# Kernel optimization log

Hardware: AMD Instinct MI355X
Metric: run time of the kernel (lower is better)

## Reference

```python
import jax, jax.numpy as jnp
import numpy as np
import math

K = 20; M = 10; N = K * M; DEG = N - 1; AJR = 30; HID = 96
NH = 4; HD = HID + 2 + K; DM = NH * HD  # 472


def _graph():
    # complete graph: node i receives edges from all j != i (fixed in-degree DEG)
    idx = jnp.arange(N)
    j = jnp.arange(DEG)
    srcs = jnp.where(j[None, :] < idx[:, None], j[None, :], j[None, :] + 1)  # [N, DEG]
    grp = idx // M
    same = (grp[srcs] == grp[:, None]).astype(jnp.float32)  # e_type[:,1]
    return srcs, same


def _pe_table(max_step, dim):
    pos = np.arange(max_step)[:, None].astype(np.float32)
    div = np.exp(np.arange(0, dim, 2).astype(np.float32) * -(math.log(10000.0) / dim))
    pe = np.zeros((max_step, dim), np.float32)
    pe[:, 0::2] = np.sin(pos * div)
    pe[:, 1::2] = np.cos(pos * div)
    return jnp.asarray(pe)


def _gcn(h, x, label, w, d, srcs, same, p):
    (l0w, l0b, l1w, l1b, l2w, l2b, l3w, l3b, l4w, l4b, l5w, l5b) = p
    t0 = 1.0 - same
    h_src = h[srcs]                      # [N, DEG, HID] gather
    we = w[..., None]
    n1_v = (h_src * we * t0[..., None]).sum(1) / (w * t0).sum(1, keepdims=True)
    n2_v = (h_src * we * same[..., None]).sum(1) / (w * same).sum(1, keepdims=True)
    n1_e = jnp.sort(d * t0, axis=1)[:, ::-1][:, :AJR]      # top-AJR cross-group dists
    n2_e = jnp.sort(d * same, axis=1)[:, ::-1][:, :M - 1]  # top-(m-1) same-group dists
    return jax.nn.relu(x @ l0w + l0b + label @ l1w + l1b + n1_v @ l2w + l2b
                       + n2_v @ l3w + l3b + n1_e @ l4w + l4b + n2_e @ l5w + l5b)


def _forward(x, label, h0, w, d,
             l0_w, l0_b, l1_w, l1_b, l2_w, l2_b, l3_w, l3_b, l4_w, l4_b, l5_w, l5_b,
             mha_w0, mha_b0, mha_w1, mha_b1, mha_w3, mha_b3,
             v1_w, v1_b, v2_w, v2_b, gnn_step, max_step, remain_step):
    srcs, same = _graph()
    gcn_p = (l0_w, l0_b, l1_w, l1_b, l2_w, l2_b, l3_w, l3_b, l4_w, l4_b, l5_w, l5_b)
    h = h0
    for _ in range(gnn_step):
        h = _gcn(h, x, label, w, d, srcs, same, gcn_p)
    pe = _pe_table(max_step, HID)
    h_full = jnp.concatenate([h + pe[remain_step], x, label], axis=1)  # [N, HD]
    gc = h_full.T @ label / M                                          # [HD, K]
    kv = jnp.tile(h_full, (1, NH))                                     # [N, DM]
    kh = (kv @ mha_w0 + mha_b0).reshape(N, NH, HD).transpose(1, 0, 2)  # keys use linears[0]
    vh = (kv @ mha_w1 + mha_b1).reshape(N, NH, HD).transpose(1, 0, 2)  # values use linears[1]
    h_rep = jnp.repeat(h_full, N, axis=0)      # torch repeat(1,n).view(n*n, hd)
    h_tile = jnp.tile(h_full, (N, 1))          # torch repeat(n,1)
    la_rep = jnp.repeat(label, N, axis=0) @ gc.T
    la_tile = jnp.tile(label, (N, 1)) @ gc.T
    Q1 = jnp.concatenate([h_rep, h_tile, la_rep, la_tile], axis=1)  # [N*N, DM]
    Q2 = jnp.concatenate([h_tile, h_rep, la_tile, la_rep], axis=1)
    inv_sqrt_dk = 1.0 / jnp.sqrt(jnp.float32(HD))

    def attend(Q):
        q = (Q @ mha_w0 + mha_b0).reshape(-1, NH, HD)
        s = jnp.einsum('bhd,hkd->bhk', q, kh) * inv_sqrt_dk
        p = jax.nn.softmax(s, axis=-1)
        o = jnp.einsum('bhk,hkd->bhd', p, vh).reshape(-1, DM)
        return o @ mha_w3 + mha_b3

    S = attend(Q1) + attend(Q2)               # [N*N, DM]
    S_a_encoding = S[:, None, :]              # [N*N, 1, DM]
    Q_sa = (jax.nn.relu(S @ v1_w + v1_b) @ v2_w + v2_b).squeeze()  # [N*N]
    return S_a_encoding, h, h_full, Q_sa


def setup_inputs() -> dict:
    key = jax.random.key(0)
    ks = jax.random.split(key, 32)
    def rn(i, shape, s=1.0):
        return jax.random.normal(ks[i], shape, jnp.float32) * s
    grp = jnp.arange(N) // M
    label = jax.nn.one_hot(grp, K, dtype=jnp.float32)
    return {
        'x': rn(0, (N, 2)),
        'label': label,
        'h0': rn(1, (N, HID)),
        'w': jax.random.uniform(ks[2], (N, DEG), jnp.float32, 0.1, 1.0),
        'd': jax.random.uniform(ks[3], (N, DEG), jnp.float32, 0.0, 1.0),
        'l0_w': rn(4, (2, HID), 0.5), 'l0_b': rn(5, (HID,), 0.05),
        'l1_w': rn(6, (K, HID), 0.2), 'l1_b': rn(7, (HID,), 0.05),
        'l2_w': rn(8, (HID, HID), 0.1), 'l2_b': rn(9, (HID,), 0.05),
        'l3_w': rn(10, (HID, HID), 0.1), 'l3_b': rn(11, (HID,), 0.05),
        'l4_w': rn(12, (AJR, HID), 0.15), 'l4_b': rn(13, (HID,), 0.05),
        'l5_w': rn(14, (M - 1, HID), 0.3), 'l5_b': rn(15, (HID,), 0.05),
        'mha_w0': rn(16, (DM, DM), 0.04), 'mha_b0': rn(17, (DM,), 0.02),
        'mha_w1': rn(18, (DM, DM), 0.04), 'mha_b1': rn(19, (DM,), 0.02),
        'mha_w3': rn(20, (DM, DM), 0.04), 'mha_b3': rn(21, (DM,), 0.02),
        'v1_w': rn(22, (DM, HID // 2), 0.04), 'v1_b': rn(23, (HID // 2,), 0.02),
        'v2_w': rn(24, (HID // 2, 1), 0.1), 'v2_b': rn(25, (1,), 0.02),
        'gnn_step': 2, 'max_step': 50, 'remain_step': 10,
    }


def reference(x, label, h0, w, d,
              l0_w, l0_b, l1_w, l1_b, l2_w, l2_b, l3_w, l3_b, l4_w, l4_b, l5_w, l5_b,
              mha_w0, mha_b0, mha_w1, mha_b1, mha_w3, mha_b3,
              v1_w, v1_b, v2_w, v2_b, gnn_step, max_step, remain_step):
    return _forward(x, label, h0, w, d,
                    l0_w, l0_b, l1_w, l1_b, l2_w, l2_b, l3_w, l3_b, l4_w, l4_b, l5_w, l5_b,
                    mha_w0, mha_b0, mha_w1, mha_b1, mha_w3, mha_b3,
                    v1_w, v1_b, v2_w, v2_b, gnn_step, max_step, remain_step)
```

## Files before the change

kernel.cpp:

```cpp
#include <hip/hip_runtime.h>
#include <hip/hip_bf16.h>
#include <math.h>

typedef unsigned short ushort;
typedef unsigned int uint;

#define NV 200
#define DEG 199
#define HID 96
#define KG 20
#define MG 10
#define AJR 30
#define NH 4
#define HD 118
#define DM 472
#define NN 40000
#define NT 20100
#define NTP 20160

#define WS_BASE   0
#define WS_H1     19200
#define WS_H2     38400
#define WS_HFULL  57600
#define WS_GMEAN  81200
#define WS_KHF    194952
#define WS_VHF    289352
#define WS_B1     383752
#define WS_B2     478152
#define WS_SC1    572552
#define WS_SC2    732552
#define WS_ZT     1315464

#define OFF_H   18880000
#define OFF_HF  18899200
#define OFF_Q   18922800

typedef __attribute__((ext_vector_type(8))) short short8v;
typedef __attribute__((ext_vector_type(4))) float float4v;

__device__ __forceinline__ ushort f2bf(float f) {
  uint u = __float_as_uint(f);
  uint r = (u + 0x7fffu + ((u >> 16) & 1u)) >> 16;
  return (ushort)r;
}
__device__ __forceinline__ uint packbf(float a, float b) {
  __hip_bfloat162 h2 = __float22bfloat162_rn(make_float2(a, b));
  union { __hip_bfloat162 h; uint u; } c;
  c.h = h2;
  return c.u;
}

__device__ __forceinline__ int triOff(int i) {
  return i * 200 - ((i * (i - 1)) >> 1);
}
__device__ __forceinline__ void p2ij(int p, int& io, int& jo) {
  float s = sqrtf((float)(160801 - 8 * p));
  int i = (int)((401.0f - s) * 0.5f);
  if (i < 0) i = 0;
  if (i > 199) i = 199;
  while (i > 0 && triOff(i) > p) --i;
  while (i < 199 && triOff(i + 1) <= p) ++i;
  io = i;
  jo = i + (p - triOff(i));
}

__global__ __launch_bounds__(256) void k_base(
    const float* __restrict__ x, const float* __restrict__ dmat,
    const float* __restrict__ label,
    const float* __restrict__ l0w, const float* __restrict__ l0b,
    const float* __restrict__ l1w, const float* __restrict__ l1b,
    const float* __restrict__ l2b, const float* __restrict__ l3b,
    const float* __restrict__ l4w, const float* __restrict__ l4b,
    const float* __restrict__ l5w, const float* __restrict__ l5b,
    float* __restrict__ base) {
  int i = blockIdx.x; int t = threadIdx.x;
  int g = i / MG;
  __shared__ float sv[256];
  __shared__ float sn2[9];
  float v = -1.0f;
  if (t < DEG) {
    int u = (t < i) ? t : t + 1;
    if (u / MG != g) v = dmat[i * DEG + t];
  }
  sv[t] = v;
  __syncthreads();
  for (int k2 = 2; k2 <= 256; k2 <<= 1) {
    for (int jj = k2 >> 1; jj > 0; jj >>= 1) {
      int ixj = t ^ jj;
      if (ixj > t) {
        float a = sv[t], b = sv[ixj];
        bool sw = ((t & k2) == 0) ? (a < b) : (a > b);
        if (sw) { sv[t] = b; sv[ixj] = a; }
      }
      __syncthreads();
    }
  }
  if (t == 0) {
    float tmp[9];
    for (int q = 0; q < 9; q++) tmp[q] = dmat[i * DEG + MG * g + q];
    for (int a2 = 1; a2 < 9; a2++) {
      float key = tmp[a2]; int b2 = a2 - 1;
      while (b2 >= 0 && tmp[b2] < key) { tmp[b2 + 1] = tmp[b2]; b2--; }
      tmp[b2 + 1] = key;
    }
    for (int q = 0; q < 9; q++) sn2[q] = tmp[q];
  }
  __syncthreads();
  if (t < HID) {
    float acc = l0b[t] + l1b[t] + l2b[t] + l3b[t] + l4b[t] + l5b[t];
    acc += x[i * 2 + 0] * l0w[t] + x[i * 2 + 1] * l0w[HID + t];
    for (int k = 0; k < KG; k++) acc += label[i * KG + k] * l1w[k * HID + t];
    for (int q = 0; q < AJR; q++) acc += sv[q] * l4w[q * HID + t];
    for (int q = 0; q < 9; q++) acc += sn2[q] * l5w[q * HID + t];
    base[i * HID + t] = acc;
  }
}

__global__ __launch_bounds__(256) void k_gcn2(
    const float* __restrict__ hin, const float* __restrict__ base,
    const float* __restrict__ w, const float* __restrict__ l2w,
    const float* __restrict__ l3w, float* __restrict__ hout) {
  int i = blockIdx.x; int t = threadIdx.x;
  int g = i / MG;
  __shared__ float pA[HID], wA[HID], pB[HID], wB[HID];
  __shared__ float n1s[HID], n2s[HID];
  __shared__ float m0[HID], m1[HID];
  if (t < HID) {
    float acc = 0.f, ws = 0.f;
    for (int j = 0; j < 100; j++) {
      int u = (j < i) ? j : j + 1;
      if (u / MG != g) {
        float wj = w[i * DEG + j];
        acc += wj * hin[u * HID + t];
        ws += wj;
      }
    }
    pA[t] = acc; wA[t] = ws;
  } else if (t < 2 * HID) {
    int dd = t - HID;
    float acc = 0.f, ws = 0.f;
    for (int j = 100; j < DEG; j++) {
      int u = (j < i) ? j : j + 1;
      if (u / MG != g) {
        float wj = w[i * DEG + j];
        acc += wj * hin[u * HID + dd];
        ws += wj;
      }
    }
    pB[dd] = acc; wB[dd] = ws;
  } else if (t < 224) {
#pragma unroll
    for (int q = 0; q < 3; q++) {
      int dd = (t - 192) * 3 + q;
      float acc = 0.f, ws = 0.f;
      for (int u = MG * g; u < MG * g + MG; u++) {
        if (u == i) continue;
        int j = (u < i) ? u : u - 1;
        float wj = w[i * DEG + j];
        acc += wj * hin[u * HID + dd];
        ws += wj;
      }
      n2s[dd] = acc / ws;
    }
  }
  __syncthreads();
  if (t < HID) n1s[t] = (pA[t] + pB[t]) / (wA[t] + wB[t]);
  __syncthreads();
  if (t < HID) {
    float acc = 0.f;
    for (int dd = 0; dd < 48; dd++)
      acc += n1s[dd] * l2w[dd * HID + t] + n2s[dd] * l3w[dd * HID + t];
    m0[t] = acc;
  } else if (t < 2 * HID) {
    int c = t - HID;
    float acc = 0.f;
    for (int dd = 48; dd < HID; dd++)
      acc += n1s[dd] * l2w[dd * HID + c] + n2s[dd] * l3w[dd * HID + c];
    m1[c] = acc;
  }
  __syncthreads();
  if (t < HID)
    hout[i * HID + t] = fmaxf(base[i * HID + t] + m0[t] + m1[t], 0.f);
}

__global__ __launch_bounds__(128) void k_hfull(
    const float* __restrict__ h, const float* __restrict__ x,
    const float* __restrict__ label, const int* __restrict__ remain_step,
    float* __restrict__ hfull, float* __restrict__ out_h,
    float* __restrict__ out_hf) {
  int i = blockIdx.x; int t = threadIdx.x;
  if (t < HD) {
    float v;
    if (t < HID) {
      int p = *remain_step;
      int t2 = t & ~1;
      float div = expf(-(float)t2 * (logf(10000.f) / (float)HID));
      float ang = (float)p * div;
      float pe = (t & 1) ? cosf(ang) : sinf(ang);
      float hv = h[i * HID + t];
      out_h[i * HID + t] = hv;
      v = hv + pe;
    } else if (t < HID + 2) {
      v = x[i * 2 + (t - HID)];
    } else {
      v = label[i * KG + (t - HID - 2)];
    }
    hfull[i * HD + t] = v;
    out_hf[i * HD + t] = v;
  }
}

__global__ __launch_bounds__(128) void k_gmean(
    const float* __restrict__ hfull, float* __restrict__ gmean) {
  int g = blockIdx.x; int t = threadIdx.x;
  if (t < HD) {
    float s = 0.f;
    for (int q = 0; q < MG; q++) s += hfull[(g * MG + q) * HD + t];
    gmean[g * HD + t] = s * 0.1f;
  }
}

__global__ __launch_bounds__(256) void k_kvB(
    const float* __restrict__ hfull, const float* __restrict__ gmean,
    const float* __restrict__ w0, const float* __restrict__ b0v,
    const float* __restrict__ w1, const float* __restrict__ b1v,
    float* __restrict__ khfT, float* __restrict__ vhf,
    float* __restrict__ B1, float* __restrict__ B2) {
  int i = blockIdx.x; int t = threadIdx.x; int g = i / MG;
  int half = blockIdx.y;
  __shared__ float hr[HD], gr[HD];
  if (t < HD) { hr[t] = hfull[i * HD + t]; gr[t] = gmean[g * HD + t]; }
  __syncthreads();
  for (int c = half * 236 + t; c < 236 + half * 236; c += 256) {
    const float* w0c = w0 + c;
    const float* w1c = w1 + c;
    float d0 = 0.f, d1 = 0.f, d2 = 0.f, d3 = 0.f;
    float g2 = 0.f, g3 = 0.f;
    float e0 = 0.f, e1 = 0.f, e2 = 0.f, e3 = 0.f;
    for (int dd = 0; dd < HD; dd++) {
      float hv = hr[dd], gv = gr[dd];
      float a0 = w0c[dd * DM];
      float a1 = w0c[(HD + dd) * DM];
      float a2 = w0c[(2 * HD + dd) * DM];
      float a3 = w0c[(3 * HD + dd) * DM];
      d0 += hv * a0; d1 += hv * a1; d2 += hv * a2; d3 += hv * a3;
      g2 += gv * a2; g3 += gv * a3;
      e0 += hv * w1c[dd * DM];
      e1 += hv * w1c[(HD + dd) * DM];
      e2 += hv * w1c[(2 * HD + dd) * DM];
      e3 += hv * w1c[(3 * HD + dd) * DM];
    }
    float b0c = b0v[c];
    khfT[c * NV + i] = b0c + d0 + d1 + d2 + d3;
    vhf[i * DM + c] = b1v[c] + e0 + e1 + e2 + e3;
    B1[i * DM + c] = d0 + g2;
    B2[i * DM + c] = b0c + d1 + g3;
  }
}

__global__ __launch_bounds__(256) void k_SC(
    const float* __restrict__ B1, const float* __restrict__ B2,
    const float* __restrict__ khfT, float* __restrict__ SC1,
    float* __restrict__ SC2) {
  int i = blockIdx.x; int t = threadIdx.x;
  int half = blockIdx.y;
  const float scl = 1.4426950408889634f / sqrtf((float)HD);
  __shared__ float b1r[DM], b2r[DM];
  for (int c = t; c < DM; c += 256) { b1r[c] = B1[i * DM + c]; b2r[c] = B2[i * DM + c]; }
  __syncthreads();
  for (int p = half * 400 + t; p < half * 400 + 400; p += 256) {
    int h = p / NV, k = p - h * NV;
    float s1a = 0.f, s2a = 0.f;
    const float* kc = khfT + (size_t)h * HD * NV + k;
    const float* b1h = b1r + h * HD;
    const float* b2h = b2r + h * HD;
    for (int dd = 0; dd < HD; dd++) {
      float kv = kc[dd * NV];
      s1a += b1h[dd] * kv;
      s2a += b2h[dd] * kv;
    }
    SC1[h * NN + i * NV + k] = s1a * scl;
    SC2[h * NN + i * NV + k] = s2a * scl;
  }
}

__global__ __launch_bounds__(256) void k_ml(
    const float* __restrict__ SC1, const float* __restrict__ SC2,
    float* __restrict__ C) {
  int i = blockIdx.x, h = blockIdx.y;
  int t = threadIdx.x;
  __shared__ float s1s[224];
  for (int k = t; k < 224; k += 256)
    s1s[k] = (k < NV) ? SC1[h * NN + i * NV + k] : -1e30f;
  __syncthreads();
  int l = t & 31;
  int g = t >> 5;
  const float* s2b = SC2 + h * NN;
  for (int it = 0; it < 25; ++it) {
    int j = it * 8 + g;
    const float* row = s2b + j * NV;
    float v[7];
#pragma unroll
    for (int e = 0; e < 7; ++e) {
      int k = l + 32 * e;
      v[e] = (k < NV) ? (s1s[k] + row[k]) : -1e30f;
    }
    float m = v[0];
#pragma unroll
    for (int e = 1; e < 7; ++e) m = fmaxf(m, v[e]);
#pragma unroll
    for (int off = 16; off > 0; off >>= 1) m = fmaxf(m, __shfl_xor(m, off, 32));
    float s = 0.f;
#pragma unroll
    for (int e = 0; e < 7; ++e) s += exp2f(v[e] - m);
#pragma unroll
    for (int off = 16; off > 0; off >>= 1) s += __shfl_xor(s, off, 32);
    if (l == 0) C[h * NN + i * NV + j] = m + log2f(s);
  }
}

__global__ __launch_bounds__(256) void k_ZZT(
    const float* __restrict__ vhf, const float* __restrict__ w3,
    ushort* __restrict__ ZT) {
  int k = blockIdx.x, h = blockIdx.y;
  int t = threadIdx.x;
  __shared__ float vr[HD];
  if (k < NV && t < HD) vr[t] = vhf[k * DM + h * HD + t];
  __syncthreads();
  for (int c = t; c < 512; c += 256) {
    float a = 0.f;
    if (k < NV && c < DM) {
      for (int d = 0; d < HD; ++d) a += vr[d] * w3[(h * HD + d) * DM + c];
    }
    ZT[(size_t)c * 896 + h * 224 + k] = f2bf(a);
  }
}

__global__ __launch_bounds__(256) void k_sfusedT2(
    const float* __restrict__ SC1, const float* __restrict__ SC2,
    const float* __restrict__ C, const ushort* __restrict__ ZT,
    const float* __restrict__ b3, float* __restrict__ outS) {
  int t = threadIdx.x;
  int c0 = blockIdx.x * 128, p0 = blockIdx.y * 64;
  int lane = t & 63, wm = t >> 6;
  int frow = lane & 15, quad = lane >> 4;
  __shared__ __align__(16) ushort Bs[128 * 40];
  int p = p0 + wm * 16 + frow;
  bool bval = (p < NT);
  int iA = 0, jA = 0;
  if (bval) p2ij(p, iA, jA);
  int iN = iA * NV, jN = jA * NV;
  float4v acc[8];
#pragma unroll
  for (int n = 0; n < 8; ++n) acc[n] = (float4v)(0.f);
  int rB = t >> 1, khB = (t & 1) * 16;

  for (int h = 0; h < NH; ++h) {
    int hb = h * NN;
    const float* s1h = SC1 + hb;
    const float* s2h = SC2 + hb;
    float ci = bval ? C[hb + iN + jA] : 0.f;
    float cj = bval ? C[hb + jN + iA] : 0.f;
    for (int ks = 0; ks < 7; ++ks) {
      int kb = ks * 32 + quad * 8;
      bool kvalid = (kb + 7 < NV);
      union { uint4 q; short8v v; } af;
      if (bval && kvalid) {
        const float* q1i = s1h + iN + kb;
        const float* q2i = s2h + iN + kb;
        const float* q1j = s1h + jN + kb;
        const float* q2j = s2h + jN + kb;
        float4 a0 = *(const float4*)q1i,   a0b = *(const float4*)(q1i + 4);
        float4 b0 = *(const float4*)q2j,   b0b = *(const float4*)(q2j + 4);
        float4 d0 = *(const float4*)q1j,   d0b = *(const float4*)(q1j + 4);
        float4 e0 = *(const float4*)q2i,   e0b = *(const float4*)(q2i + 4);
        float p0_ = exp2f(a0.x + b0.x - ci) + exp2f(d0.x + e0.x - cj);
        float p1_ = exp2f(a0.y + b0.y - ci) + exp2f(d0.y + e0.y - cj);
        float p2_ = exp2f(a0.z + b0.z - ci) + exp2f(d0.z + e0.z - cj);
        float p3_ = exp2f(a0.w + b0.w - ci) + exp2f(d0.w + e0.w - cj);
        float p4_ = exp2f(a0b.x + b0b.x - ci) + exp2f(d0b.x + e0b.x - cj);
        float p5_ = exp2f(a0b.y + b0b.y - ci) + exp2f(d0b.y + e0b.y - cj);
        float p6_ = exp2f(a0b.z + b0b.z - ci) + exp2f(d0b.z + e0b.z - cj);
        float p7_ = exp2f(a0b.w + b0b.w - ci) + exp2f(d0b.w + e0b.w - cj);
        af.q.x = packbf(p0_, p1_);
        af.q.y = packbf(p2_, p3_);
        af.q.z = packbf(p4_, p5_);
        af.q.w = packbf(p6_, p7_);
      } else {
        af.q = make_uint4(0, 0, 0, 0);
      }
      const uint4* wp = (const uint4*)(ZT + (size_t)(c0 + rB) * 896 +
                                       h * 224 + ks * 32 + khB);
      uint4 bq0 = wp[0], bq1 = wp[1];
      __syncthreads();
      *(uint4*)&Bs[rB * 40 + khB] = bq0;
      *(uint4*)&Bs[rB * 40 + khB + 8] = bq1;
      __syncthreads();
#pragma unroll
      for (int n = 0; n < 8; ++n) {
        short8v bf = *(const short8v*)&Bs[(n * 16 + frow) * 40 + quad * 8];
        acc[n] = __builtin_amdgcn_mfma_f32_16x16x32_bf16(af.v, bf, acc[n],
                                                         0, 0, 0);
      }
    }
  }
  int ie[4], je[4];
#pragma unroll
  for (int r2 = 0; r2 < 4; ++r2) {
    int pe = p0 + wm * 16 + quad * 4 + r2;
    if (pe < NT) {
      p2ij(pe, ie[r2], je[r2]);
    } else {
      ie[r2] = -1; je[r2] = 0;
    }
  }
#pragma unroll
  for (int n = 0; n < 8; ++n) {
    int c = c0 + n * 16 + frow;
    if (c >= DM) continue;
    float bb = 2.0f * b3[c];
#pragma unroll
    for (int r2 = 0; r2 < 4; ++r2) {
      int ii = ie[r2];
      if (ii < 0) continue;
      int jj = je[r2];
      float v = acc[n][r2] + bb;
      outS[(size_t)(ii * NV + jj) * DM + c] = v;
      if (ii != jj) outS[(size_t)(jj * NV + ii) * DM + c] = v;
    }
  }
}

__global__ __launch_bounds__(256) void k_qsaT2(
    const float* __restrict__ S, const float* __restrict__ v1w,
    const float* __restrict__ v1b, const float* __restrict__ v2w,
    const float* __restrict__ v2b, float* __restrict__ outQ) {
  __shared__ float Ss[32][61];
  __shared__ float V1s[59][48];
  __shared__ float Ts[32][49];
  __shared__ int rowI[32], rowJ[32], rowOfs[32];
  int t = threadIdx.x;
  int p0b = blockIdx.x * 32;
  if (t < 32) {
    int p = p0b + t;
    if (p < NT) {
      int ii, jj; p2ij(p, ii, jj);
      rowI[t] = ii; rowJ[t] = jj; rowOfs[t] = ii * NV + jj;
    } else {
      rowI[t] = -1; rowJ[t] = 0; rowOfs[t] = 0;
    }
  }
  int ty2 = (t >> 4) * 2;
  int tx3 = (t & 15) * 3;
  float a00 = 0.f, a01 = 0.f, a02 = 0.f, a10 = 0.f, a11 = 0.f, a12 = 0.f;
  for (int k0 = 0; k0 < DM; k0 += 59) {
    __syncthreads();
    for (int e = t; e < 32 * 59; e += 256) {
      int r = e / 59, cc = e - r * 59;
      Ss[r][cc] = S[(size_t)rowOfs[r] * DM + k0 + cc];
    }
    for (int e = t; e < 59 * 48; e += 256) {
      int kk = e / 48, cc = e - kk * 48;
      V1s[kk][cc] = v1w[(size_t)(k0 + kk) * 48 + cc];
    }
    __syncthreads();
    for (int kk = 0; kk < 59; ++kk) {
      float s0 = Ss[ty2][kk], s1 = Ss[ty2 + 1][kk];
      float w0_ = V1s[kk][tx3], w1_ = V1s[kk][tx3 + 1], w2_ = V1s[kk][tx3 + 2];
      a00 += s0 * w0_; a01 += s0 * w1_; a02 += s0 * w2_;
      a10 += s1 * w0_; a11 += s1 * w1_; a12 += s1 * w2_;
    }
  }
  float b0 = v1b[tx3], b1 = v1b[tx3 + 1], b2 = v1b[tx3 + 2];
  Ts[ty2][tx3] = fmaxf(a00 + b0, 0.f);
  Ts[ty2][tx3 + 1] = fmaxf(a01 + b1, 0.f);
  Ts[ty2][tx3 + 2] = fmaxf(a02 + b2, 0.f);
  Ts[ty2 + 1][tx3] = fmaxf(a10 + b0, 0.f);
  Ts[ty2 + 1][tx3 + 1] = fmaxf(a11 + b1, 0.f);
  Ts[ty2 + 1][tx3 + 2] = fmaxf(a12 + b2, 0.f);
  __syncthreads();
  if (t < 32 && rowI[t] >= 0) {
    float q = v2b[0];
    for (int c = 0; c < 48; c++) q += Ts[t][c] * v2w[c];
    int ii = rowI[t], jj = rowJ[t];
    outQ[ii * NV + jj] = q;
    if (ii != jj) outQ[jj * NV + ii] = q;
  }
}

extern "C" void kernel_launch(void* const* d_in, const int* in_sizes, int n_in,
                              void* d_out, int out_size, void* d_ws,
                              size_t ws_size, hipStream_t stream) {
  const float* x = (const float*)d_in[0];
  const float* label = (const float*)d_in[1];
  const float* h0 = (const float*)d_in[2];
  const float* w = (const float*)d_in[3];
  const float* dmat = (const float*)d_in[4];
  const float* l0w = (const float*)d_in[5];
  const float* l0b = (const float*)d_in[6];
  const float* l1w = (const float*)d_in[7];
  const float* l1b = (const float*)d_in[8];
  const float* l2w = (const float*)d_in[9];
  const float* l2b = (const float*)d_in[10];
  const float* l3w = (const float*)d_in[11];
  const float* l3b = (const float*)d_in[12];
  const float* l4w = (const float*)d_in[13];
  const float* l4b = (const float*)d_in[14];
  const float* l5w = (const float*)d_in[15];
  const float* l5b = (const float*)d_in[16];
  const float* w0 = (const float*)d_in[17];
  const float* b0v = (const float*)d_in[18];
  const float* w1 = (const float*)d_in[19];
  const float* b1v = (const float*)d_in[20];
  const float* w3 = (const float*)d_in[21];
  const float* b3 = (const float*)d_in[22];
  const float* v1w = (const float*)d_in[23];
  const float* v1b = (const float*)d_in[24];
  const float* v2w = (const float*)d_in[25];
  const float* v2b = (const float*)d_in[26];
  const int* remain_step = (const int*)d_in[29];

  float* ws = (float*)d_ws;
  float* base = ws + WS_BASE;
  float* h1 = ws + WS_H1;
  float* h2 = ws + WS_H2;
  float* hfull = ws + WS_HFULL;
  float* gmean = ws + WS_GMEAN;
  float* khfT = ws + WS_KHF;
  float* vhf = ws + WS_VHF;
  float* B1 = ws + WS_B1;
  float* B2 = ws + WS_B2;
  float* SC1 = ws + WS_SC1;
  float* SC2 = ws + WS_SC2;
  ushort* ZT = (ushort*)(ws + WS_ZT);
  float* C = ws + WS_B1;

  float* outS = (float*)d_out;
  float* outH = outS + OFF_H;
  float* outHF = outS + OFF_HF;
  float* outQ = outS + OFF_Q;

  k_base<<<NV, 256, 0, stream>>>(x, dmat, label, l0w, l0b, l1w, l1b, l2b, l3b,
                                 l4w, l4b, l5w, l5b, base);
  k_gcn2<<<NV, 256, 0, stream>>>(h0, base, w, l2w, l3w, h1);
  k_gcn2<<<NV, 256, 0, stream>>>(h1, base, w, l2w, l3w, h2);
  k_hfull<<<NV, 128, 0, stream>>>(h2, x, label, remain_step, hfull, outH, outHF);
  k_gmean<<<KG, 128, 0, stream>>>(hfull, gmean);
  k_kvB<<<dim3(NV, 2), 256, 0, stream>>>(hfull, gmean, w0, b0v, w1, b1v, khfT,
                                         vhf, B1, B2);
  k_ZZT<<<dim3(224, NH), 256, 0, stream>>>(vhf, w3, ZT);
  k_SC<<<dim3(NV, 2), 256, 0, stream>>>(B1, B2, khfT, SC1, SC2);
  k_ml<<<dim3(NV, NH), 256, 0, stream>>>(SC1, SC2, C);
  k_sfusedT2<<<dim3(4, NTP / 64), 256, 0, stream>>>(SC1, SC2, C, ZT, b3, outS);
  k_qsaT2<<<(NT + 31) / 32, 256, 0, stream>>>(outS, v1w, v1b, v2w, v2b, outQ);
}
```

Baseline: 507.3 us.

## Widen fused attention-output tile and raise parallelism in small GCN/score kernels

The fused MFMA kernel now covers 256 output columns per block instead of 128. This halves how often each block recomputes the exp2-based bf16 probability A-fragments, at the cost of more accumulator registers and a larger shared tile. The GCN neighbour aggregation is split across 4 thread groups with 512-thread blocks. k_SC and k_ml get twice as many blocks by splitting their work ranges. The separate group-mean kernel is folded into k_kvB, which saves one launch but makes each block redundantly sum 10 rows.

```diff
diff --git a/kernel.cpp b/kernel.cpp
--- a/kernel.cpp
+++ b/kernel.cpp
@@ -22,7 +22,6 @@
 #define WS_H1     19200
 #define WS_H2     38400
 #define WS_HFULL  57600
-#define WS_GMEAN  81200
 #define WS_KHF    194952
 #define WS_VHF    289352
 #define WS_B1     383752
@@ -116,42 +115,33 @@
   }
 }
 
-__global__ __launch_bounds__(256) void k_gcn2(
+__global__ __launch_bounds__(512) void k_gcn4(
     const float* __restrict__ hin, const float* __restrict__ base,
     const float* __restrict__ w, const float* __restrict__ l2w,
     const float* __restrict__ l3w, float* __restrict__ hout) {
   int i = blockIdx.x; int t = threadIdx.x;
   int g = i / MG;
-  __shared__ float pA[HID], wA[HID], pB[HID], wB[HID];
+  __shared__ float pJ[4][HID], wJ[4][HID];
   __shared__ float n1s[HID], n2s[HID];
-  __shared__ float m0[HID], m1[HID];
-  if (t < HID) {
+  __shared__ float m[4][HID];
+  if (t < 384) {
+    int q = t / HID;
+    int c = t - q * HID;
+    int j0 = q * 50, j1 = (q == 3) ? DEG : (j0 + 50);
     float acc = 0.f, ws = 0.f;
-    for (int j = 0; j < 100; j++) {
+    for (int j = j0; j < j1; j++) {
       int u = (j < i) ? j : j + 1;
       if (u / MG != g) {
         float wj = w[i * DEG + j];
-        acc += wj * hin[u * HID + t];
+        acc += wj * hin[u * HID + c];
         ws += wj;
       }
     }
-    pA[t] = acc; wA[t] = ws;
-  } else if (t < 2 * HID) {
-    int dd = t - HID;
-    float acc = 0.f, ws = 0.f;
-    for (int j = 100; j < DEG; j++) {
-      int u = (j < i) ? j : j + 1;
-      if (u / MG != g) {
-        float wj = w[i * DEG + j];
-        acc += wj * hin[u * HID + dd];
-        ws += wj;
-      }
-    }
-    pB[dd] = acc; wB[dd] = ws;
-  } else if (t < 224) {
-#pragma unroll
-    for (int q = 0; q < 3; q++) {
-      int dd = (t - 192) * 3 + q;
+    pJ[q][c] = acc; wJ[q][c] = ws;
+  } else if (t < 416) {
+#pragma unroll
+    for (int q2 = 0; q2 < 3; q2++) {
+      int dd = (t - 384) * 3 + q2;
       float acc = 0.f, ws = 0.f;
       for (int u = MG * g; u < MG * g + MG; u++) {
         if (u == i) continue;
@@ -164,23 +154,22 @@
     }
   }
   __syncthreads();
-  if (t < HID) n1s[t] = (pA[t] + pB[t]) / (wA[t] + wB[t]);
-  __syncthreads();
-  if (t < HID) {
+  if (t < HID)
+    n1s[t] = (pJ[0][t] + pJ[1][t] + pJ[2][t] + pJ[3][t]) /
+             (wJ[0][t] + wJ[1][t] + wJ[2][t] + wJ[3][t]);
+  __syncthreads();
+  if (t < 384) {
+    int q = t / HID, c = t - q * HID;
+    int d0 = q * 24;
     float acc = 0.f;
-    for (int dd = 0; dd < 48; dd++)
-      acc += n1s[dd] * l2w[dd * HID + t] + n2s[dd] * l3w[dd * HID + t];
-    m0[t] = acc;
-  } else if (t < 2 * HID) {
-    int c = t - HID;
-    float acc = 0.f;
-    for (int dd = 48; dd < HID; dd++)
+    for (int dd = d0; dd < d0 + 24; dd++)
       acc += n1s[dd] * l2w[dd * HID + c] + n2s[dd] * l3w[dd * HID + c];
-    m1[c] = acc;
+    m[q][c] = acc;
   }
   __syncthreads();
   if (t < HID)
-    hout[i * HID + t] = fmaxf(base[i * HID + t] + m0[t] + m1[t], 0.f);
+    hout[i * HID + t] =
+        fmaxf(base[i * HID + t] + m[0][t] + m[1][t] + m[2][t] + m[3][t], 0.f);
 }
 
 __global__ __launch_bounds__(128) void k_hfull(
@@ -210,18 +199,8 @@
   }
 }
 
-__global__ __launch_bounds__(128) void k_gmean(
-    const float* __restrict__ hfull, float* __restrict__ gmean) {
-  int g = blockIdx.x; int t = threadIdx.x;
-  if (t < HD) {
-    float s = 0.f;
-    for (int q = 0; q < MG; q++) s += hfull[(g * MG + q) * HD + t];
-    gmean[g * HD + t] = s * 0.1f;
-  }
-}
-
 __global__ __launch_bounds__(256) void k_kvB(
-    const float* __restrict__ hfull, const float* __restrict__ gmean,
+    const float* __restrict__ hfull,
     const float* __restrict__ w0, const float* __restrict__ b0v,
     const float* __restrict__ w1, const float* __restrict__ b1v,
     float* __restrict__ khfT, float* __restrict__ vhf,
@@ -229,7 +208,12 @@
   int i = blockIdx.x; int t = threadIdx.x; int g = i / MG;
   int half = blockIdx.y;
   __shared__ float hr[HD], gr[HD];
-  if (t < HD) { hr[t] = hfull[i * HD + t]; gr[t] = gmean[g * HD + t]; }
+  if (t < HD) {
+    hr[t] = hfull[i * HD + t];
+    float s = 0.f;
+    for (int q = 0; q < MG; q++) s += hfull[(g * MG + q) * HD + t];
+    gr[t] = s * 0.1f;
+  }
   __syncthreads();
   for (int c = half * 236 + t; c < 236 + half * 236; c += 256) {
     const float* w0c = w0 + c;
@@ -263,12 +247,12 @@
     const float* __restrict__ khfT, float* __restrict__ SC1,
     float* __restrict__ SC2) {
   int i = blockIdx.x; int t = threadIdx.x;
-  int half = blockIdx.y;
+  int qtr = blockIdx.y;
   const float scl = 1.4426950408889634f / sqrtf((float)HD);
   __shared__ float b1r[DM], b2r[DM];
   for (int c = t; c < DM; c += 256) { b1r[c] = B1[i * DM + c]; b2r[c] = B2[i * DM + c]; }
   __syncthreads();
-  for (int p = half * 400 + t; p < half * 400 + 400; p += 256) {
+  for (int p = qtr * 200 + t; p < qtr * 200 + 200; p += 256) {
     int h = p / NV, k = p - h * NV;
     float s1a = 0.f, s2a = 0.f;
     const float* kc = khfT + (size_t)h * HD * NV + k;
@@ -287,7 +271,8 @@
 __global__ __launch_bounds__(256) void k_ml(
     const float* __restrict__ SC1, const float* __restrict__ SC2,
     float* __restrict__ C) {
-  int i = blockIdx.x, h = blockIdx.y;
+  int i = blockIdx.x;
+  int h = blockIdx.y >> 1, jh = blockIdx.y & 1;
   int t = threadIdx.x;
   __shared__ float s1s[224];
   for (int k = t; k < 224; k += 256)
@@ -296,7 +281,8 @@
   int l = t & 31;
   int g = t >> 5;
   const float* s2b = SC2 + h * NN;
-  for (int it = 0; it < 25; ++it) {
+  int it0 = jh ? 13 : 0, it1 = jh ? 25 : 13;
+  for (int it = it0; it < it1; ++it) {
     int j = it * 8 + g;
     const float* row = s2b + j * NV;
     float v[7];
@@ -336,24 +322,23 @@
   }
 }
 
-__global__ __launch_bounds__(256) void k_sfusedT2(
+__global__ __launch_bounds__(256) void k_sfusedT3(
     const float* __restrict__ SC1, const float* __restrict__ SC2,
     const float* __restrict__ C, const ushort* __restrict__ ZT,
     const float* __restrict__ b3, float* __restrict__ outS) {
   int t = threadIdx.x;
-  int c0 = blockIdx.x * 128, p0 = blockIdx.y * 64;
+  int c0 = blockIdx.x * 256, p0 = blockIdx.y * 64;
   int lane = t & 63, wm = t >> 6;
   int frow = lane & 15, quad = lane >> 4;
-  __shared__ __align__(16) ushort Bs[128 * 40];
+  __shared__ __align__(16) ushort Bs[256 * 40];
   int p = p0 + wm * 16 + frow;
   bool bval = (p < NT);
   int iA = 0, jA = 0;
   if (bval) p2ij(p, iA, jA);
   int iN = iA * NV, jN = jA * NV;
-  float4v acc[8];
-#pragma unroll
-  for (int n = 0; n < 8; ++n) acc[n] = (float4v)(0.f);
-  int rB = t >> 1, khB = (t & 1) * 16;
+  float4v acc[16];
+#pragma unroll
+  for (int n = 0; n < 16; ++n) acc[n] = (float4v)(0.f);
 
   for (int h = 0; h < NH; ++h) {
     int hb = h * NN;
@@ -364,6 +349,15 @@
     for (int ks = 0; ks < 7; ++ks) {
       int kb = ks * 32 + quad * 8;
       bool kvalid = (kb + 7 < NV);
+      uint4 bq[4];
+#pragma unroll
+      for (int qq = 0; qq < 4; ++qq) {
+        int li = qq * 256 + t;
+        int c = li >> 2;
+        int ko = (li & 3) * 8;
+        bq[qq] = *(const uint4*)(ZT + (size_t)(c0 + c) * 896 + h * 224 +
+                                 ks * 32 + ko);
+      }
       union { uint4 q; short8v v; } af;
       if (bval && kvalid) {
         const float* q1i = s1h + iN + kb;
@@ -389,18 +383,22 @@
       } else {
         af.q = make_uint4(0, 0, 0, 0);
       }
-      const uint4* wp = (const uint4*)(ZT + (size_t)(c0 + rB) * 896 +
-                                       h * 224 + ks * 32 + khB);
-      uint4 bq0 = wp[0], bq1 = wp[1];
       __syncthreads();
-      *(uint4*)&Bs[rB * 40 + khB] = bq0;
-      *(uint4*)&Bs[rB * 40 + khB + 8] = bq1;
+#pragma unroll
+      for (int qq = 0; qq < 4; ++qq) {
+        int li = qq * 256 + t;
+        int c = li >> 2;
+        int ko = (li & 3) * 8;
+        *(uint4*)&Bs[c * 40 + ko] = bq[qq];
+      }
       __syncthreads();
 #pragma unroll
-      for (int n = 0; n < 8; ++n) {
-        short8v bf = *(const short8v*)&Bs[(n * 16 + frow) * 40 + quad * 8];
-        acc[n] = __builtin_amdgcn_mfma_f32_16x16x32_bf16(af.v, bf, acc[n],
-                                                         0, 0, 0);
+      for (int n = 0; n < 16; ++n) {
+        if (c0 + n * 16 < DM) {
+          short8v bf = *(const short8v*)&Bs[(n * 16 + frow) * 40 + quad * 8];
+          acc[n] = __builtin_amdgcn_mfma_f32_16x16x32_bf16(af.v, bf, acc[n],
+                                                           0, 0, 0);
+        }
       }
     }
   }
@@ -415,7 +413,7 @@
     }
   }
 #pragma unroll
-  for (int n = 0; n < 8; ++n) {
+  for (int n = 0; n < 16; ++n) {
     int c = c0 + n * 16 + frow;
     if (c >= DM) continue;
     float bb = 2.0f * b3[c];
@@ -525,7 +523,6 @@
   float* h1 = ws + WS_H1;
   float* h2 = ws + WS_H2;
   float* hfull = ws + WS_HFULL;
-  float* gmean = ws + WS_GMEAN;
   float* khfT = ws + WS_KHF;
   float* vhf = ws + WS_VHF;
   float* B1 = ws + WS_B1;
@@ -542,15 +539,14 @@
 
   k_base<<<NV, 256, 0, stream>>>(x, dmat, label, l0w, l0b, l1w, l1b, l2b, l3b,
                                  l4w, l4b, l5w, l5b, base);
-  k_gcn2<<<NV, 256, 0, stream>>>(h0, base, w, l2w, l3w, h1);
-  k_gcn2<<<NV, 256, 0, stream>>>(h1, base, w, l2w, l3w, h2);
+  k_gcn4<<<NV, 512, 0, stream>>>(h0, base, w, l2w, l3w, h1);
+  k_gcn4<<<NV, 512, 0, stream>>>(h1, base, w, l2w, l3w, h2);
   k_hfull<<<NV, 128, 0, stream>>>(h2, x, label, remain_step, hfull, outH, outHF);
-  k_gmean<<<KG, 128, 0, stream>>>(hfull, gmean);
-  k_kvB<<<dim3(NV, 2), 256, 0, stream>>>(hfull, gmean, w0, b0v, w1, b1v, khfT,
-                                         vhf, B1, B2);
+  k_kvB<<<dim3(NV, 2), 256, 0, stream>>>(hfull, w0, b0v, w1, b1v, khfT, vhf,
+                                         B1, B2);
   k_ZZT<<<dim3(224, NH), 256, 0, stream>>>(vhf, w3, ZT);
-  k_SC<<<dim3(NV, 2), 256, 0, stream>>>(B1, B2, khfT, SC1, SC2);
-  k_ml<<<dim3(NV, NH), 256, 0, stream>>>(SC1, SC2, C);
-  k_sfusedT2<<<dim3(4, NTP / 64), 256, 0, stream>>>(SC1, SC2, C, ZT, b3, outS);
+  k_SC<<<dim3(NV, 4), 256, 0, stream>>>(B1, B2, khfT, SC1, SC2);
+  k_ml<<<dim3(NV, NH * 2), 256, 0, stream>>>(SC1, SC2, C);
+  k_sfusedT3<<<dim3(2, NTP / 64), 256, 0, stream>>>(SC1, SC2, C, ZT, b3, outS);
   k_qsaT2<<<(NT + 31) / 32, 256, 0, stream>>>(outS, v1w, v1b, v2w, v2b, outQ);
 }
```

Result: slower. 534.7 us (+5.4%).
